# Kernel tuning notes

Hardware: AMD Instinct MI355X
Metric: run time of the kernel (lower is better)

The kernel has to match this reference:

```python
import jax, jax.numpy as jnp
import numpy as np

N = 100000      # nodes
E = 1600000     # edges (before self-loops)
IN = 256        # in_channels
HID = 16        # num_hid (per-head channels, layer 1)
HEADS = 4
OUT = 16        # out_channels (per-head channels, layer 2)
NEG_SLOPE = 0.2 # PyG GATConv default


def setup_inputs() -> dict:
    key = jax.random.key(0)
    ks = jax.random.split(key, 12)
    def glorot(k, shape, fan):
        return jax.random.normal(k, shape, jnp.float32) * (1.0 / np.sqrt(fan))
    x = jax.random.normal(ks[0], (N, IN), jnp.float32)
    edge_index = jax.random.randint(ks[1], (2, E), 0, N, dtype=jnp.int32)
    W1 = glorot(ks[2], (IN, HEADS * HID), IN)
    att_src1 = glorot(ks[3], (HEADS, HID), HID)
    att_dst1 = glorot(ks[4], (HEADS, HID), HID)
    b1 = jnp.zeros((HEADS * HID,), jnp.float32)
    W2 = glorot(ks[5], (HEADS * HID, HEADS * OUT), HEADS * HID)
    att_src2 = glorot(ks[6], (HEADS, OUT), OUT)
    att_dst2 = glorot(ks[7], (HEADS, OUT), OUT)
    b2 = jnp.zeros((HEADS * OUT,), jnp.float32)
    return {"x": x, "edge_index": edge_index, "W1": W1, "att_src1": att_src1,
            "att_dst1": att_dst1, "b1": b1, "W2": W2, "att_src2": att_src2,
            "att_dst2": att_dst2, "b2": b2}


def gat_conv(x, W, att_src, att_dst, bias, src, dst):
    # PyG GATConv (concat=True): h = xW per head; alpha via segment-softmax over dst.
    H, C = att_src.shape
    n = x.shape[0]
    h = (x @ W).reshape(n, H, C)                    # [N,H,C]
    a_s = jnp.sum(h * att_src, axis=-1)             # [N,H]
    a_d = jnp.sum(h * att_dst, axis=-1)             # [N,H]
    e = jax.nn.leaky_relu(a_s[src] + a_d[dst], NEG_SLOPE)  # [E',H]
    m = jax.lax.stop_gradient(jax.ops.segment_max(e, dst, num_segments=n))
    p = jnp.exp(e - m[dst])
    s = jax.ops.segment_sum(p, dst, num_segments=n)
    alpha = p / (s[dst] + 1e-16)                    # [E',H]
    msg = h[src] * alpha[:, :, None]                # [E',H,C] gathered messages
    out = jax.ops.segment_sum(msg, dst, num_segments=n)
    return out.reshape(n, H * C) + bias


def reference(x, edge_index, W1, att_src1, att_dst1, b1, W2, att_src2, att_dst2, b2):
    # add self loops (PyG GATConv default add_self_loops=True)
    loops = jnp.arange(N, dtype=edge_index.dtype)
    src = jnp.concatenate([edge_index[0], loops])
    dst = jnp.concatenate([edge_index[1], loops])
    h = jax.nn.relu(gat_conv(x, W1, att_src1, att_dst1, b1, src, dst))
    # dropout is identity in eval mode
    return gat_conv(h, W2, att_src2, att_dst2, b2, src, dst)
```

## Files before the change

### kernel.cpp

```cpp
#include <hip/hip_runtime.h>
#include <hip/hip_fp16.h>
#include <cstdint>


#define CH 4096
#define MAXB 512
#define SCAP 6144

__device__ __forceinline__ float lrelu(float v) { return fmaxf(v, 0.2f * v); }

__global__ void ifill_kernel(int* __restrict__ p, int v, int n) {
  int i = blockIdx.x * blockDim.x + threadIdx.x;
  if (i < n) p[i] = v;
}

__global__ __launch_bounds__(256) void bucket_hist(const int* __restrict__ edst,
                                                   int E, int nbuck,
                                                   int* __restrict__ bucket_cnt) {
  __shared__ int hist[MAXB];
  const int t = threadIdx.x;
  for (int j = t; j < MAXB; j += 256) hist[j] = 0;
  __syncthreads();
  const int base = blockIdx.x * CH;
#pragma unroll
  for (int k = 0; k < CH / 256; ++k) {
    int e = base + k * 256 + t;
    if (e < E) atomicAdd(&hist[edst[e] >> 8], 1);
  }
  __syncthreads();
  for (int j = t; j < nbuck; j += 256) {
    int c = hist[j];
    if (c) atomicAdd(&bucket_cnt[j], c);
  }
}

__global__ __launch_bounds__(512) void bucket_scan(const int* __restrict__ bucket_cnt,
                                                   int* __restrict__ bucket_base,
                                                   int* __restrict__ bucket_cursor,
                                                   int nbuck) {
  __shared__ int part[512];
  const int t = threadIdx.x;
  int v = (t < nbuck) ? bucket_cnt[t] : 0;
  part[t] = v;
  __syncthreads();
  for (int off = 1; off < 512; off <<= 1) {
    int u = (t >= off) ? part[t - off] : 0;
    __syncthreads();
    part[t] += u;
    __syncthreads();
  }
  int ex = part[t] - v;
  if (t <= nbuck) {
    int w = (t < nbuck) ? ex : part[nbuck - 1];
    bucket_base[t] = w;
    if (t < nbuck) bucket_cursor[t] = w;
  }
}

__global__ __launch_bounds__(256) void place_kernel(const int* __restrict__ esrc,
                                                    const int* __restrict__ edst,
                                                    int E, int nbuck,
                                                    int* __restrict__ bucket_cursor,
                                                    unsigned int* __restrict__ pairs) {
  __shared__ int hist[MAXB];
  __shared__ int gbase[MAXB];
  __shared__ int rcnt[MAXB];
  const int t = threadIdx.x;
  for (int j = t; j < MAXB; j += 256) { hist[j] = 0; rcnt[j] = 0; }
  __syncthreads();
  const int base = blockIdx.x * CH;
  int b_[CH / 256];
  unsigned int p_[CH / 256];
#pragma unroll
  for (int k = 0; k < CH / 256; ++k) {
    int e = base + k * 256 + t;
    if (e < E) {
      int d = edst[e];
      int s = esrc[e];
      b_[k] = d >> 8;
      p_[k] = ((unsigned int)s << 8) | (unsigned int)(d & 255);
      atomicAdd(&hist[b_[k]], 1);
    } else {
      b_[k] = -1;
    }
  }
  __syncthreads();
  for (int j = t; j < nbuck; j += 256) {
    int c = hist[j];
    gbase[j] = c ? atomicAdd(&bucket_cursor[j], c) : 0;
  }
  __syncthreads();
#pragma unroll
  for (int k = 0; k < CH / 256; ++k) {
    if (b_[k] >= 0) {
      int r = atomicAdd(&rcnt[b_[k]], 1);
      pairs[gbase[b_[k]] + r] = p_[k];
    }
  }
}

__global__ __launch_bounds__(256) void bucket_build(
    const unsigned int* __restrict__ pairs, const int* __restrict__ bucket_base,
    int* __restrict__ ccol, int* __restrict__ start, int* __restrict__ endp,
    int n) {
  __shared__ int cnt[256];
  __shared__ int ls[256];
  __shared__ int csave[256];
  __shared__ int part[256];
  __shared__ int sorted[SCAP];
  const int t = threadIdx.x;
  const int b = blockIdx.x;
  const int d0 = b << 8;
  const int DR = min(256, n - d0);
  const int in_base = bucket_base[b];
  const int nloc = bucket_base[b + 1] - in_base;
  const int out_base = in_base + d0;

  cnt[t] = (t < DR) ? 1 : 0;
  __syncthreads();
  for (int i = t; i < nloc; i += 256)
    atomicAdd(&cnt[pairs[in_base + i] & 255u], 1);
  __syncthreads();
  int c = cnt[t];
  csave[t] = c;
  part[t] = c;
  __syncthreads();
#pragma unroll
  for (int off = 1; off < 256; off <<= 1) {
    int u = (t >= off) ? part[t - off] : 0;
    __syncthreads();
    part[t] += u;
    __syncthreads();
  }
  ls[t] = part[t] - c;
  __syncthreads();
  if (t < DR) {
    int s = out_base + ls[t];
    start[d0 + t] = s;
    endp[d0 + t] = s + csave[t];
    sorted[ls[t]] = d0 + t;
    cnt[t] = 1;
  }
  __syncthreads();
  for (int i = t; i < nloc; i += 256) {
    unsigned int p = pairs[in_base + i];
    int j = (int)(p & 255u);
    int r = atomicAdd(&cnt[j], 1);
    int pos = ls[j] + r;
    if (pos < SCAP) sorted[pos] = (int)(p >> 8);
  }
  __syncthreads();
  int tot = nloc + DR;
  if (tot > SCAP) tot = SCAP;
  for (int i = t; i < tot; i += 256) ccol[out_base + i] = sorted[i];
}

template <int K>
__global__ __launch_bounds__(256) void gemm_att(
    const float* __restrict__ x, const float* __restrict__ W,
    const float* __restrict__ att_src, const float* __restrict__ att_dst,
    __half* __restrict__ h, float* __restrict__ as_, float* __restrict__ ad_,
    int n) {
  __shared__ float xs[64 * 68];
  __shared__ float ws[64 * 64];
  const int tid = threadIdx.x;
  const int ty = tid >> 4;
  const int tx = tid & 15;
  const int row0 = blockIdx.x * 64;
  const int sr = tid >> 4;
  const int sc = tid & 15;

  float acc[4][4] = {{0.f}};

  for (int c = 0; c < K; c += 64) {
    __syncthreads();
    {
      const float4* wsrc = (const float4*)(W + (long long)c * 64);
      float4* wdst = (float4*)ws;
#pragma unroll
      for (int j = 0; j < 4; ++j) wdst[tid + j * 256] = wsrc[tid + j * 256];
    }
#pragma unroll
    for (int j = 0; j < 4; ++j) {
      int r = sr + j * 16;
      int rr = row0 + r;
      if (rr > n - 1) rr = n - 1;
      float4 v = *(const float4*)(x + (long long)rr * K + c + sc * 4);
      *(float4*)(xs + r * 68 + sc * 4) = v;
    }
    __syncthreads();
#pragma unroll 2
    for (int kk = 0; kk < 64; kk += 4) {
      float4 xv[4], wv[4];
#pragma unroll
      for (int i = 0; i < 4; ++i)
        xv[i] = *(const float4*)(xs + (ty * 4 + i) * 68 + kk);
#pragma unroll
      for (int q = 0; q < 4; ++q)
        wv[q] = *(const float4*)(ws + (kk + q) * 64 + tx * 4);
#pragma unroll
      for (int q = 0; q < 4; ++q) {
#pragma unroll
        for (int i = 0; i < 4; ++i) {
          float xq = (q == 0) ? xv[i].x : (q == 1) ? xv[i].y : (q == 2) ? xv[i].z : xv[i].w;
          acc[i][0] = fmaf(xq, wv[q].x, acc[i][0]);
          acc[i][1] = fmaf(xq, wv[q].y, acc[i][1]);
          acc[i][2] = fmaf(xq, wv[q].z, acc[i][2]);
          acc[i][3] = fmaf(xq, wv[q].w, acc[i][3]);
        }
      }
    }
  }

  const float4 atts = *(const float4*)(att_src + tx * 4);
  const float4 attd = *(const float4*)(att_dst + tx * 4);
  const int head = tx >> 2;
#pragma unroll
  for (int i = 0; i < 4; ++i) {
    int row = row0 + ty * 4 + i;
    if (row >= n) break;
    ushort4 hv;
    hv.x = __half_as_ushort(__float2half_rn(acc[i][0]));
    hv.y = __half_as_ushort(__float2half_rn(acc[i][1]));
    hv.z = __half_as_ushort(__float2half_rn(acc[i][2]));
    hv.w = __half_as_ushort(__float2half_rn(acc[i][3]));
    *(ushort4*)(h + (long long)row * 64 + tx * 4) = hv;
    float s = acc[i][0] * atts.x + acc[i][1] * atts.y + acc[i][2] * atts.z + acc[i][3] * atts.w;
    float d = acc[i][0] * attd.x + acc[i][1] * attd.y + acc[i][2] * attd.z + acc[i][3] * attd.w;
    s += __shfl_xor(s, 1);
    s += __shfl_xor(s, 2);
    d += __shfl_xor(d, 1);
    d += __shfl_xor(d, 2);
    if ((tx & 3) == 0) {
      as_[(long long)row * 4 + head] = s;
      ad_[(long long)row * 4 + head] = d;
    }
  }
}

__global__ __launch_bounds__(256) void node_agg_kernel(
    const int* __restrict__ ccol, const int* __restrict__ start,
    const int* __restrict__ endp,
    const float* __restrict__ as_, const float* __restrict__ ad_,
    const __half2* __restrict__ h2, const float* __restrict__ bias,
    float* __restrict__ out, int n, int do_relu) {
  const int node = blockIdx.x * 8 + (threadIdx.x >> 5);
  if (node >= n) return;
  const int hl = threadIdx.x & 31;
  const int hh = hl >> 3;
  const float adv = ad_[node * 4 + hh];
  const int s0i = start[node];
  const int d = endp[node] - s0i;
  const int* cp = ccol + s0i;
  float ax = 0.f, ay = 0.f, den = 0.f;
  int i = 0;
  for (; i + 4 <= d; i += 4) {
    int s0 = cp[i], s1 = cp[i + 1], s2 = cp[i + 2], s3 = cp[i + 3];
    float p0 = __expf(lrelu(as_[s0 * 4 + hh] + adv));
    float p1 = __expf(lrelu(as_[s1 * 4 + hh] + adv));
    float p2 = __expf(lrelu(as_[s2 * 4 + hh] + adv));
    float p3 = __expf(lrelu(as_[s3 * 4 + hh] + adv));
    float2 h0 = __half22float2(h2[s0 * 32 + hl]);
    float2 h1 = __half22float2(h2[s1 * 32 + hl]);
    float2 h2v = __half22float2(h2[s2 * 32 + hl]);
    float2 h3 = __half22float2(h2[s3 * 32 + hl]);
    den += (p0 + p1) + (p2 + p3);
    ax = fmaf(p0, h0.x, ax); ay = fmaf(p0, h0.y, ay);
    ax = fmaf(p1, h1.x, ax); ay = fmaf(p1, h1.y, ay);
    ax = fmaf(p2, h2v.x, ax); ay = fmaf(p2, h2v.y, ay);
    ax = fmaf(p3, h3.x, ax); ay = fmaf(p3, h3.y, ay);
  }
  for (; i < d; ++i) {
    int s0 = cp[i];
    float p0 = __expf(lrelu(as_[s0 * 4 + hh] + adv));
    float2 h0 = __half22float2(h2[s0 * 32 + hl]);
    den += p0;
    ax = fmaf(p0, h0.x, ax); ay = fmaf(p0, h0.y, ay);
  }
  const float inv = 1.0f / (den + 1e-16f);
  float vx = ax * inv + bias[hl * 2];
  float vy = ay * inv + bias[hl * 2 + 1];
  if (do_relu) { vx = fmaxf(vx, 0.f); vy = fmaxf(vy, 0.f); }
  *(float2*)(out + node * 64 + hl * 2) = make_float2(vx, vy);
}

extern "C" void kernel_launch(void* const* d_in, const int* in_sizes, int n_in,
                              void* d_out, int out_size, void* d_ws, size_t ws_size,
                              hipStream_t stream) {
  const float* x = (const float*)d_in[0];
  const int* ei = (const int*)d_in[1];
  const float* W1 = (const float*)d_in[2];
  const float* att_s1 = (const float*)d_in[3];
  const float* att_d1 = (const float*)d_in[4];
  const float* b1 = (const float*)d_in[5];
  const float* W2 = (const float*)d_in[6];
  const float* att_s2 = (const float*)d_in[7];
  const float* att_d2 = (const float*)d_in[8];
  const float* b2 = (const float*)d_in[9];

  const int n = in_sizes[0] / 256;
  const int E = in_sizes[1] / 2;
  const int* esrc = ei;
  const int* edst = ei + E;
  const int nbuck = (n + 255) >> 8;

  float* wsf = (float*)d_ws;
  __half* hbuf = (__half*)wsf;
  float* xbuf = wsf + (long long)n * 64;
  float* as_ = xbuf + (long long)n * 64;
  float* ad_ = as_ + (long long)n * 4;
  int* bucket_cnt = (int*)(ad_ + (long long)n * 4);
  int* bucket_base = bucket_cnt + MAXB;
  int* bucket_cursor = bucket_base + MAXB + 1;
  int* start = bucket_cursor + MAXB;
  int* endp = start + n;
  unsigned int* pairs = (unsigned int*)(endp + n);
  int* ccol = (int*)(pairs + E);
  float* out = (float*)d_out;

  const int ebk = (E + CH - 1) / CH;
  const int gb = (n + 63) / 64;
  const int nb = (n + 7) / 8;

  ifill_kernel<<<(MAXB + 255) / 256, 256, 0, stream>>>(bucket_cnt, 0, MAXB);
  bucket_hist<<<ebk, 256, 0, stream>>>(edst, E, nbuck, bucket_cnt);
  bucket_scan<<<1, 512, 0, stream>>>(bucket_cnt, bucket_base, bucket_cursor, nbuck);
  place_kernel<<<ebk, 256, 0, stream>>>(esrc, edst, E, nbuck, bucket_cursor, pairs);
  bucket_build<<<nbuck, 256, 0, stream>>>(pairs, bucket_base, ccol, start, endp, n);

  gemm_att<256><<<gb, 256, 0, stream>>>(x, W1, att_s1, att_d1, hbuf, as_, ad_, n);
  node_agg_kernel<<<nb, 256, 0, stream>>>(ccol, start, endp, as_, ad_,
                                          (const __half2*)hbuf, b1, xbuf, n, 1);

  gemm_att<64><<<gb, 256, 0, stream>>>(xbuf, W2, att_s2, att_d2, hbuf, as_, ad_, n);
  node_agg_kernel<<<nb, 256, 0, stream>>>(ccol, start, endp, as_, ad_,
                                          (const __half2*)hbuf, b2, out, n, 0);
}
```

Before: 227.3 us.

## Use fp16 MFMA for node GEMMs and store layer-1 activations as half

Replaces the FP32 CUDA-core tiled GEMM with a 16x16x32 fp16 MFMA kernel. The weights are pre-transposed and converted to half by a small prep kernel, and the whole weight matrix is staged in LDS. The first aggregation now writes its ReLU output as fp16, which halves the traffic read by the second GEMM. This lowers GEMM compute and memory cost but loses precision on the input x and the intermediate activations, and adds two small launches.

```diff
diff --git a/kernel.cpp b/kernel.cpp
--- a/kernel.cpp
+++ b/kernel.cpp
@@ -7,11 +7,24 @@
 #define MAXB 512
 #define SCAP 6144
 
+using f16x8 = __attribute__((ext_vector_type(8))) _Float16;
+using f16x4 = __attribute__((ext_vector_type(4))) _Float16;
+using f32x4 = __attribute__((ext_vector_type(4))) float;
+
 __device__ __forceinline__ float lrelu(float v) { return fmaxf(v, 0.2f * v); }
 
 __global__ void ifill_kernel(int* __restrict__ p, int v, int n) {
   int i = blockIdx.x * blockDim.x + threadIdx.x;
   if (i < n) p[i] = v;
+}
+
+__global__ void wprep_kernel(const float* __restrict__ W, ushort* __restrict__ WT,
+                             int K) {
+  int i = blockIdx.x * 256 + threadIdx.x;
+  if (i < K * 64) {
+    int k = i >> 6, nn = i & 63;
+    WT[nn * K + k] = __half_as_ushort(__float2half_rn(W[i]));
+  }
 }
 
 __global__ __launch_bounds__(256) void bucket_hist(const int* __restrict__ edst,
@@ -155,85 +168,86 @@
   for (int i = t; i < tot; i += 256) ccol[out_base + i] = sorted[i];
 }
 
-template <int K>
-__global__ __launch_bounds__(256) void gemm_att(
-    const float* __restrict__ x, const float* __restrict__ W,
+template <int K, bool XHALF>
+__global__ __launch_bounds__(256) void gemm_mfma(
+    const void* __restrict__ xin, const ushort* __restrict__ wt,
     const float* __restrict__ att_src, const float* __restrict__ att_dst,
     __half* __restrict__ h, float* __restrict__ as_, float* __restrict__ ad_,
     int n) {
-  __shared__ float xs[64 * 68];
-  __shared__ float ws[64 * 64];
+  constexpr int WS = K + 8;
+  __shared__ _Float16 wsh[64 * WS];
+  __shared__ _Float16 xsh[64 * 72];
   const int tid = threadIdx.x;
-  const int ty = tid >> 4;
-  const int tx = tid & 15;
+  const int w = tid >> 6;
+  const int lane = tid & 63;
+  const int lr = lane & 15;
+  const int kg = lane >> 4;
   const int row0 = blockIdx.x * 64;
-  const int sr = tid >> 4;
-  const int sc = tid & 15;
-
-  float acc[4][4] = {{0.f}};
+
+  {
+    const ushort4* src = (const ushort4*)wt;
+    for (int i4 = tid; i4 < 64 * K / 4; i4 += 256) {
+      int nr = i4 / (K / 4);
+      int kc = i4 % (K / 4);
+      *(ushort4*)&wsh[nr * WS + kc * 4] = src[i4];
+    }
+  }
+
+  f32x4 acc[4] = {};
+  const int tr = tid >> 2;
+  const int tc = (tid & 3) * 16;
+  int rr = row0 + tr;
+  if (rr > n - 1) rr = n - 1;
 
   for (int c = 0; c < K; c += 64) {
     __syncthreads();
-    {
-      const float4* wsrc = (const float4*)(W + (long long)c * 64);
-      float4* wdst = (float4*)ws;
-#pragma unroll
-      for (int j = 0; j < 4; ++j) wdst[tid + j * 256] = wsrc[tid + j * 256];
-    }
-#pragma unroll
-    for (int j = 0; j < 4; ++j) {
-      int r = sr + j * 16;
-      int rr = row0 + r;
-      if (rr > n - 1) rr = n - 1;
-      float4 v = *(const float4*)(x + (long long)rr * K + c + sc * 4);
-      *(float4*)(xs + r * 68 + sc * 4) = v;
-    }
-    __syncthreads();
-#pragma unroll 2
-    for (int kk = 0; kk < 64; kk += 4) {
-      float4 xv[4], wv[4];
-#pragma unroll
-      for (int i = 0; i < 4; ++i)
-        xv[i] = *(const float4*)(xs + (ty * 4 + i) * 68 + kk);
-#pragma unroll
-      for (int q = 0; q < 4; ++q)
-        wv[q] = *(const float4*)(ws + (kk + q) * 64 + tx * 4);
-#pragma unroll
-      for (int q = 0; q < 4; ++q) {
-#pragma unroll
-        for (int i = 0; i < 4; ++i) {
-          float xq = (q == 0) ? xv[i].x : (q == 1) ? xv[i].y : (q == 2) ? xv[i].z : xv[i].w;
-          acc[i][0] = fmaf(xq, wv[q].x, acc[i][0]);
-          acc[i][1] = fmaf(xq, wv[q].y, acc[i][1]);
-          acc[i][2] = fmaf(xq, wv[q].z, acc[i][2]);
-          acc[i][3] = fmaf(xq, wv[q].w, acc[i][3]);
-        }
+    if constexpr (!XHALF) {
+      const float* xp = (const float*)xin + (long long)rr * K + c + tc;
+#pragma unroll
+      for (int j = 0; j < 4; ++j) {
+        float4 v = *(const float4*)(xp + j * 4);
+        f16x4 hv;
+        hv[0] = (_Float16)v.x; hv[1] = (_Float16)v.y;
+        hv[2] = (_Float16)v.z; hv[3] = (_Float16)v.w;
+        *(f16x4*)&xsh[tr * 72 + tc + j * 4] = hv;
       }
-    }
-  }
-
-  const float4 atts = *(const float4*)(att_src + tx * 4);
-  const float4 attd = *(const float4*)(att_dst + tx * 4);
-  const int head = tx >> 2;
-#pragma unroll
-  for (int i = 0; i < 4; ++i) {
-    int row = row0 + ty * 4 + i;
-    if (row >= n) break;
-    ushort4 hv;
-    hv.x = __half_as_ushort(__float2half_rn(acc[i][0]));
-    hv.y = __half_as_ushort(__float2half_rn(acc[i][1]));
-    hv.z = __half_as_ushort(__float2half_rn(acc[i][2]));
-    hv.w = __half_as_ushort(__float2half_rn(acc[i][3]));
-    *(ushort4*)(h + (long long)row * 64 + tx * 4) = hv;
-    float s = acc[i][0] * atts.x + acc[i][1] * atts.y + acc[i][2] * atts.z + acc[i][3] * atts.w;
-    float d = acc[i][0] * attd.x + acc[i][1] * attd.y + acc[i][2] * attd.z + acc[i][3] * attd.w;
-    s += __shfl_xor(s, 1);
-    s += __shfl_xor(s, 2);
-    d += __shfl_xor(d, 1);
-    d += __shfl_xor(d, 2);
-    if ((tx & 3) == 0) {
-      as_[(long long)row * 4 + head] = s;
-      ad_[(long long)row * 4 + head] = d;
+    } else {
+      const ushort* xp = (const ushort*)xin + (long long)rr * K + c + tc;
+#pragma unroll
+      for (int j = 0; j < 4; ++j)
+        *(ushort4*)&xsh[tr * 72 + tc + j * 4] = *(const ushort4*)(xp + j * 4);
+    }
+    __syncthreads();
+#pragma unroll
+    for (int ks = 0; ks < 64; ks += 32) {
+      f16x8 a = *(const f16x8*)&xsh[(w * 16 + lr) * 72 + ks + kg * 8];
+#pragma unroll
+      for (int ct = 0; ct < 4; ++ct) {
+        f16x8 b = *(const f16x8*)&wsh[(ct * 16 + lr) * WS + c + ks + kg * 8];
+        acc[ct] = __builtin_amdgcn_mfma_f32_16x16x32_f16(a, b, acc[ct], 0, 0, 0);
+      }
+    }
+  }
+
+  const int wrow = row0 + w * 16 + kg * 4;
+#pragma unroll
+  for (int ct = 0; ct < 4; ++ct) {
+    const float as0 = att_src[ct * 16 + lr];
+    const float ad0 = att_dst[ct * 16 + lr];
+#pragma unroll
+    for (int r = 0; r < 4; ++r) {
+      const int row = wrow + r;
+      const float v = acc[ct][r];
+      if (row < n) h[(long long)row * 64 + ct * 16 + lr] = __float2half_rn(v);
+      float s = v * as0, d = v * ad0;
+      s += __shfl_xor(s, 1); s += __shfl_xor(s, 2);
+      s += __shfl_xor(s, 4); s += __shfl_xor(s, 8);
+      d += __shfl_xor(d, 1); d += __shfl_xor(d, 2);
+      d += __shfl_xor(d, 4); d += __shfl_xor(d, 8);
+      if (lr == 0 && row < n) {
+        as_[row * 4 + ct] = s;
+        ad_[row * 4 + ct] = d;
+      }
     }
   }
 }
@@ -243,7 +257,7 @@
     const int* __restrict__ endp,
     const float* __restrict__ as_, const float* __restrict__ ad_,
     const __half2* __restrict__ h2, const float* __restrict__ bias,
-    float* __restrict__ out, int n, int do_relu) {
+    float* __restrict__ fout, __half2* __restrict__ hout, int n, int mode) {
   const int node = blockIdx.x * 8 + (threadIdx.x >> 5);
   if (node >= n) return;
   const int hl = threadIdx.x & 31;
@@ -280,8 +294,13 @@
   const float inv = 1.0f / (den + 1e-16f);
   float vx = ax * inv + bias[hl * 2];
   float vy = ay * inv + bias[hl * 2 + 1];
-  if (do_relu) { vx = fmaxf(vx, 0.f); vy = fmaxf(vy, 0.f); }
-  *(float2*)(out + node * 64 + hl * 2) = make_float2(vx, vy);
+  if (mode == 1) {
+    vx = fmaxf(vx, 0.f);
+    vy = fmaxf(vy, 0.f);
+    hout[node * 32 + hl] = __floats2half2_rn(vx, vy);
+  } else {
+    *(float2*)(fout + node * 64 + hl * 2) = make_float2(vx, vy);
+  }
 }
 
 extern "C" void kernel_launch(void* const* d_in, const int* in_sizes, int n_in,
@@ -316,11 +335,16 @@
   int* endp = start + n;
   unsigned int* pairs = (unsigned int*)(endp + n);
   int* ccol = (int*)(pairs + E);
+  ushort* wt1 = (ushort*)(((uintptr_t)(ccol + E + n) + 15) & ~(uintptr_t)15);
+  ushort* wt2 = wt1 + 64 * 256;
   float* out = (float*)d_out;
 
   const int ebk = (E + CH - 1) / CH;
   const int gb = (n + 63) / 64;
   const int nb = (n + 7) / 8;
+
+  wprep_kernel<<<(256 * 64 + 255) / 256, 256, 0, stream>>>(W1, wt1, 256);
+  wprep_kernel<<<(64 * 64 + 255) / 256, 256, 0, stream>>>(W2, wt2, 64);
 
   ifill_kernel<<<(MAXB + 255) / 256, 256, 0, stream>>>(bucket_cnt, 0, MAXB);
   bucket_hist<<<ebk, 256, 0, stream>>>(edst, E, nbuck, bucket_cnt);
@@ -328,11 +352,15 @@
   place_kernel<<<ebk, 256, 0, stream>>>(esrc, edst, E, nbuck, bucket_cursor, pairs);
   bucket_build<<<nbuck, 256, 0, stream>>>(pairs, bucket_base, ccol, start, endp, n);
 
-  gemm_att<256><<<gb, 256, 0, stream>>>(x, W1, att_s1, att_d1, hbuf, as_, ad_, n);
+  gemm_mfma<256, false><<<gb, 256, 0, stream>>>(x, wt1, att_s1, att_d1,
+                                                hbuf, as_, ad_, n);
   node_agg_kernel<<<nb, 256, 0, stream>>>(ccol, start, endp, as_, ad_,
-                                          (const __half2*)hbuf, b1, xbuf, n, 1);
-
-  gemm_att<64><<<gb, 256, 0, stream>>>(xbuf, W2, att_s2, att_d2, hbuf, as_, ad_, n);
+                                          (const __half2*)hbuf, b1,
+                                          nullptr, (__half2*)xbuf, n, 1);
+
+  gemm_mfma<64, true><<<gb, 256, 0, stream>>>(xbuf, wt2, att_s2, att_d2,
+                                              hbuf, as_, ad_, n);
   node_agg_kernel<<<nb, 256, 0, stream>>>(ccol, start, endp, as_, ad_,
-                                          (const __half2*)hbuf, b2, out, n, 0);
-}
+                                          (const __half2*)hbuf, b2,
+                                          out, nullptr, n, 0);
+}
```

Measured after the change: 229.0 us. Within noise of the previous version (+0.7%).
